# Kernel optimization log

Hardware: AMD Instinct MI355X
Metric: run time of the kernel (lower is better)

## Reference

```python
import jax, jax.numpy as jnp
import numpy as np

H = 8  # n_heads from init_kwargs
EPS = 1e-5


def _ln(x, g, b):
    m = jnp.mean(x, axis=-1, keepdims=True)
    v = jnp.mean((x - m) ** 2, axis=-1, keepdims=True)
    return (x - m) * jax.lax.rsqrt(v + EPS) * g + b


def setup_inputs() -> dict:
    key = jax.random.key(0)
    B, d_m, n, L, p_d = 1, 256, 128, 1024, 128
    ks = jax.random.split(key, 12)
    s = 0.02
    return {
        "msa": jax.random.normal(ks[0], (B, d_m, n, L), jnp.float32),
        "pairs": jax.random.normal(ks[1], (B, n, n, p_d), jnp.float32),
        "ln_m_g": jnp.ones((d_m,), jnp.float32),
        "ln_m_b": jnp.zeros((d_m,), jnp.float32),
        "ln_p_g": jnp.ones((p_d,), jnp.float32),
        "ln_p_b": jnp.zeros((p_d,), jnp.float32),
        "Wq": jax.random.normal(ks[2], (d_m, d_m), jnp.float32) * s,
        "Wk": jax.random.normal(ks[3], (d_m, d_m), jnp.float32) * s,
        "Wv": jax.random.normal(ks[4], (d_m, d_m), jnp.float32) * s,
        "Wg": jax.random.normal(ks[5], (d_m, d_m), jnp.float32) * s,
        "bg": jnp.zeros((d_m,), jnp.float32),
        "Wb": jax.random.normal(ks[6], (p_d, H), jnp.float32) * s,
        "Wo": jax.random.normal(ks[7], (d_m, d_m), jnp.float32) * s,
        "bo": jnp.zeros((d_m,), jnp.float32),
    }


def reference(msa, pairs, ln_m_g, ln_m_b, ln_p_g, ln_p_b,
              Wq, Wk, Wv, Wg, bg, Wb, Wo, bo):
    B, d_m, n, L = msa.shape
    dh = d_m // H
    sqrt_c = jnp.sqrt(jnp.asarray(dh, msa.dtype))

    x = _ln(jnp.transpose(msa, (0, 3, 2, 1)), ln_m_g, ln_m_b)      # [B,L,n,d_m]
    p = _ln(pairs, ln_p_g, ln_p_b)                                   # [B,n,n,p_d]

    # pair bias: (B,n,n,H) -> (B,1,H,n_q,n_k)
    bias = jnp.transpose(jnp.einsum('bijc,ch->bijh', p, Wb), (0, 3, 1, 2))[:, None]

    def heads(y):  # [B,L,n,d_m] -> [B,L,H,n,dh]
        return jnp.transpose(y.reshape(B, L, n, H, dh), (0, 1, 3, 2, 4))

    q = heads(x @ Wq)
    k = heads(x @ Wk)
    v = heads(x @ Wv)
    g = jax.nn.sigmoid(heads(x @ Wg + bg))

    scores = jnp.einsum('blhnd,blhmd->blhnm', q, k) / sqrt_c + bias  # [B,L,H,n,n]
    w = jax.nn.softmax(scores, axis=-1)
    attn = g * jnp.einsum('blhnm,blhmd->blhnd', w, v)                # [B,L,H,n,dh]

    attn = jnp.transpose(attn, (0, 1, 3, 2, 4)).reshape(B, L, n, d_m)
    out = attn @ Wo + bo                                             # [B,L,n,d_m]
    return jnp.transpose(out, (0, 3, 2, 1))                          # [B,d_m,n,L]
```

## Files before the change

kernel.cpp:

```cpp
#include <hip/hip_runtime.h>

__device__ __forceinline__ float bf_lo(unsigned u){ return __uint_as_float(u << 16); }
__device__ __forceinline__ float bf_hi(unsigned u){ return __uint_as_float(u & 0xffff0000u); }
__device__ __forceinline__ float bf1(unsigned short s){ return __uint_as_float((unsigned)s << 16); }
__device__ __forceinline__ unsigned short f2bf(float f){
  unsigned u = __float_as_uint(f);
  u += 0x7fffu + ((u >> 16) & 1u);
  return (unsigned short)(u >> 16);
}

typedef __attribute__((ext_vector_type(8))) short short8;
typedef __attribute__((ext_vector_type(4))) float f32x4;

__device__ __forceinline__ f32x4 mfma16(short8 a, short8 b, f32x4 c){
  return __builtin_amdgcn_mfma_f32_16x16x32_bf16(a, b, c, 0, 0, 0);
}

#define GLOAD_LDS16(g, l) \
  __builtin_amdgcn_global_load_lds((const __attribute__((address_space(1))) unsigned int*)(g), \
                                   (__attribute__((address_space(3))) unsigned int*)(l), 16, 0, 0)

__global__ __launch_bounds__(256) void ln_msa_kernel(
    const float* __restrict__ msa, const float* __restrict__ gam,
    const float* __restrict__ bet, unsigned short* __restrict__ x16)
{
  __shared__ float tile[256*33];
  __shared__ float ps[8*32], pq[8*32];
  __shared__ float mean_s[32], rstd_s[32];
  const int t = threadIdx.x;
  const int l0 = blockIdx.x * 32;
  const int n  = blockIdx.y;
  {
    const int lt = t & 31, ct = t >> 5;
    for (int r = 0; r < 32; ++r) {
      int c = r*8 + ct;
      tile[c*33 + lt] = msa[(size_t)c*131072 + (size_t)n*1024 + l0 + lt];
    }
  }
  __syncthreads();
  {
    const int lt = t & 31, cp = t >> 5;
    float s1 = 0.f, s2 = 0.f;
    for (int cc = 0; cc < 32; ++cc) {
      int c = cp*32 + ((cc + cp*4) & 31);
      float v = tile[c*33 + lt];
      s1 += v; s2 += v*v;
    }
    ps[cp*32 + lt] = s1; pq[cp*32 + lt] = s2;
  }
  __syncthreads();
  if (t < 32) {
    float s1 = 0.f, s2 = 0.f;
    for (int cp = 0; cp < 8; ++cp){ s1 += ps[cp*32+t]; s2 += pq[cp*32+t]; }
    float m = s1 * (1.f/256.f);
    float v = s2 * (1.f/256.f) - m*m;
    mean_s[t] = m;
    rstd_s[t] = rsqrtf(v + 1e-5f);
  }
  __syncthreads();
  {
    const float g = gam[t], b = bet[t];
    for (int l = 0; l < 32; ++l) {
      float v = (tile[t*33 + l] - mean_s[l]) * rstd_s[l] * g + b;
      x16[((size_t)(l0+l)*128 + n)*256 + t] = f2bf(v);
    }
  }
}

__global__ __launch_bounds__(64) void pair_bias_kernel(
    const float* __restrict__ pairs, const float* __restrict__ gam,
    const float* __restrict__ bet, const float* __restrict__ Wb,
    float* __restrict__ biasb)
{
  const int j = blockIdx.x, i = blockIdx.y;
  const int t = threadIdx.x;
  const float* row = pairs + ((size_t)i*128 + j)*128;
  float v0 = row[t], v1 = row[t+64];
  float s = v0 + v1;
  #pragma unroll
  for (int o = 1; o < 64; o <<= 1) s += __shfl_xor(s, o, 64);
  float m = s * (1.f/128.f);
  float d0 = v0 - m, d1 = v1 - m;
  float q = d0*d0 + d1*d1;
  #pragma unroll
  for (int o = 1; o < 64; o <<= 1) q += __shfl_xor(q, o, 64);
  float rstd = rsqrtf(q * (1.f/128.f) + 1e-5f);
  float n0 = d0 * rstd * gam[t]    + bet[t];
  float n1 = d1 * rstd * gam[t+64] + bet[t+64];
  #pragma unroll
  for (int h = 0; h < 8; ++h) {
    float p = n0 * Wb[t*8 + h] + n1 * Wb[(t+64)*8 + h];
    #pragma unroll
    for (int o = 1; o < 64; o <<= 1) p += __shfl_xor(p, o, 64);
    if (t == h) biasb[((size_t)h*128 + i)*128 + j] = p;
  }
}

__global__ __launch_bounds__(256) void wprep_kernel(
    const float* __restrict__ Wq, const float* __restrict__ Wk,
    const float* __restrict__ Wv, const float* __restrict__ Wg,
    const float* __restrict__ Wo,
    unsigned short* __restrict__ Wt, unsigned short* __restrict__ WoT)
{
  const int n = blockIdx.x, k = threadIdx.x;
  if (n < 1024) {
    const int mat = n >> 8, nl = n & 255;
    const float* W = (mat==0) ? Wq : (mat==1) ? Wk : (mat==2) ? Wv : Wg;
    float v = W[(size_t)k*256 + nl];
    if (mat == 0) v *= 0.17677669529663689f;
    Wt[(size_t)n*256 + k] = f2bf(v);
  } else {
    const int c = n - 1024;
    WoT[(size_t)c*256 + k] = f2bf(Wo[(size_t)k*256 + c]);
  }
}

__global__ __launch_bounds__(256) void qkvg_gemm(
    const unsigned short* __restrict__ X, const unsigned short* __restrict__ Wt,
    const float* __restrict__ bg, unsigned short* __restrict__ qkg,
    unsigned short* __restrict__ vT)
{
  __shared__ __align__(16) unsigned short As[128*64], Bs[128*64];
  const int t = threadIdx.x;
  const int m0 = blockIdx.x*128, n0 = blockIdx.y*128;
  const int w = t>>6, lane = t&63, fr = lane&15, quad = lane>>4;
  const int wm = (w>>1)*64, wn = (w&1)*64;
  f32x4 acc[4][4] = {};
  for (int k0 = 0; k0 < 256; k0 += 64) {
    if (k0) __syncthreads();
    #pragma unroll
    for (int pss = 0; pss < 4; ++pss) {
      int s = pss*256 + t;
      int row = s >> 3, pch = s & 7;
      int c = pch ^ (row & 7);
      const unsigned short* ga = X  + (size_t)(m0+row)*256 + k0 + c*8;
      const unsigned short* gb = Wt + (size_t)(n0+row)*256 + k0 + c*8;
      GLOAD_LDS16(ga, As + (s & ~63)*8);
      GLOAD_LDS16(gb, Bs + (s & ~63)*8);
    }
    __syncthreads();
    #pragma unroll
    for (int kt = 0; kt < 2; ++kt) {
      short8 af[4], bfr[4];
      #pragma unroll
      for (int mt=0;mt<4;++mt){ int r = wm+mt*16+fr; int ch = (kt*4+quad)^(r&7);
        af[mt] = *(const short8*)(As + r*64 + ch*8); }
      #pragma unroll
      for (int nt=0;nt<4;++nt){ int r = wn+nt*16+fr; int ch = (kt*4+quad)^(r&7);
        bfr[nt] = *(const short8*)(Bs + r*64 + ch*8); }
      #pragma unroll
      for (int mt=0;mt<4;++mt)
        #pragma unroll
        for (int nt=0;nt<4;++nt)
          acc[mt][nt] = mfma16(af[mt], bfr[nt], acc[mt][nt]);
    }
  }
  const int mat = n0 >> 8;
  #pragma unroll
  for (int mt=0;mt<4;++mt) {
    #pragma unroll
    for (int nt=0;nt<4;++nt) {
      const int ng = n0 + wn + nt*16 + fr;
      const int h = (ng>>5)&7, d = ng&31;
      #pragma unroll
      for (int reg=0;reg<4;++reg) {
        const int m = m0 + wm + mt*16 + quad*4 + reg;
        float v = acc[mt][nt][reg];
        if (mat == 3) v = 1.f/(1.f + __expf(-(v + bg[ng&255])));
        const unsigned short bv = f2bf(v);
        if (mat == 2) {
          const int ll = m>>7, nn = m&127;
          const int c = nn>>3, ph = c ^ (d&7);
          vT[((size_t)(h*1024 + ll))*4096 + d*128 + ph*8 + (nn&7)] = bv;
        } else {
          const int mi = ((mat==3)?2:mat)*8 + h;
          qkg[((size_t)mi*131072 + m)*32 + d] = bv;
        }
      }
    }
  }
}

__global__ __launch_bounds__(512) void attn_mfma(
    const unsigned short* __restrict__ qkg, const unsigned short* __restrict__ vT,
    const float* __restrict__ biasb, unsigned short* __restrict__ attn2)
{
  __shared__ __align__(16) unsigned short qs[128*32], ks[128*32], gs[128*32], vs[32*128];
  __shared__ __align__(16) unsigned short pbuf[8][16*136];
  const int t = threadIdx.x, l = blockIdx.x;
  const int w = t>>6, fr = t&15, quad = (t>>4)&3;
  unsigned short* pw = pbuf[w];
  const int rbase = w*16;
  const f32x4 zero4 = {0.f,0.f,0.f,0.f};
  for (int h = 0; h < 8; ++h) {
    {
      const unsigned short* g0 = qkg + ((size_t)(0*8+h)*131072 + (size_t)l*128)*32 + t*8;
      const unsigned short* g1 = qkg + ((size_t)(1*8+h)*131072 + (size_t)l*128)*32 + t*8;
      const unsigned short* g2 = qkg + ((size_t)(2*8+h)*131072 + (size_t)l*128)*32 + t*8;
      const unsigned short* g3 = vT  + ((size_t)(h*1024 + l))*4096 + t*8;
      const int lb = (t & ~63)*8;
      GLOAD_LDS16(g0, qs + lb);
      GLOAD_LDS16(g1, ks + lb);
      GLOAD_LDS16(g2, gs + lb);
      GLOAD_LDS16(g3, vs + lb);
    }
    __syncthreads();
    short8 aq = *(const short8*)(qs + (rbase+fr)*32 + quad*8);
    f32x4 S[8];
    #pragma unroll
    for (int nt=0;nt<8;++nt) {
      short8 bk = *(const short8*)(ks + (nt*16+fr)*32 + quad*8);
      S[nt] = mfma16(aq, bk, zero4);
    }
    const float* bb = biasb + ((size_t)h*128 + rbase + quad*4)*128 + fr;
    #pragma unroll
    for (int nt=0;nt<8;++nt)
      #pragma unroll
      for (int reg=0;reg<4;++reg)
        S[nt][reg] += bb[(size_t)reg*128 + nt*16];
    float mx[4] = {-1e30f,-1e30f,-1e30f,-1e30f};
    #pragma unroll
    for (int nt=0;nt<8;++nt)
      #pragma unroll
      for (int reg=0;reg<4;++reg) mx[reg] = fmaxf(mx[reg], S[nt][reg]);
    #pragma unroll
    for (int reg=0;reg<4;++reg) {
      mx[reg] = fmaxf(mx[reg], __shfl_xor(mx[reg], 1, 64));
      mx[reg] = fmaxf(mx[reg], __shfl_xor(mx[reg], 2, 64));
      mx[reg] = fmaxf(mx[reg], __shfl_xor(mx[reg], 4, 64));
      mx[reg] = fmaxf(mx[reg], __shfl_xor(mx[reg], 8, 64));
    }
    float sum[4] = {0.f,0.f,0.f,0.f};
    #pragma unroll
    for (int nt=0;nt<8;++nt)
      #pragma unroll
      for (int reg=0;reg<4;++reg) {
        float e = __expf(S[nt][reg]-mx[reg]);
        S[nt][reg] = e; sum[reg] += e;
      }
    #pragma unroll
    for (int reg=0;reg<4;++reg) {
      sum[reg] += __shfl_xor(sum[reg], 1, 64);
      sum[reg] += __shfl_xor(sum[reg], 2, 64);
      sum[reg] += __shfl_xor(sum[reg], 4, 64);
      sum[reg] += __shfl_xor(sum[reg], 8, 64);
    }
    float inv[4];
    #pragma unroll
    for (int reg=0;reg<4;++reg) inv[reg] = 1.f/sum[reg];
    #pragma unroll
    for (int nt=0;nt<8;++nt)
      #pragma unroll
      for (int reg=0;reg<4;++reg)
        pw[(quad*4+reg)*136 + nt*16 + fr] = f2bf(S[nt][reg]*inv[reg]);
    __builtin_amdgcn_s_waitcnt(0);
    f32x4 o[2] = {zero4, zero4};
    #pragma unroll
    for (int kt=0;kt<4;++kt) {
      short8 ap = *(const short8*)(pw + fr*136 + kt*32 + quad*8);
      #pragma unroll
      for (int n2=0;n2<2;++n2) {
        const int d = n2*16 + fr;
        const int ph = (kt*4+quad) ^ (d&7);
        short8 bv = *(const short8*)(vs + d*128 + ph*8);
        o[n2] = mfma16(ap, bv, o[n2]);
      }
    }
    #pragma unroll
    for (int n2=0;n2<2;++n2)
      #pragma unroll
      for (int reg=0;reg<4;++reg) {
        const int row = rbase + quad*4 + reg, col = n2*16 + fr;
        const float gv = bf1(gs[row*32 + col]);
        attn2[((size_t)row*1024 + l)*256 + h*32 + col] = f2bf(o[n2][reg]*gv);
      }
    __syncthreads();
  }
}

__global__ __launch_bounds__(256) void outproj_mfma(
    const unsigned short* __restrict__ attn2, const unsigned short* __restrict__ WoT,
    const float* __restrict__ bo, float* __restrict__ out)
{
  __shared__ __align__(16) unsigned short As[128*64], Bs[128*64];
  const int t = threadIdx.x;
  const int c0 = blockIdx.x*128;
  const int l0 = blockIdx.y*128;
  const int n  = blockIdx.z;
  const int w = t>>6, lane = t&63, fr = lane&15, quad = lane>>4;
  const int wm = (w>>1)*64, wn = (w&1)*64;
  f32x4 acc[4][4] = {};
  for (int k0 = 0; k0 < 256; k0 += 64) {
    if (k0) __syncthreads();
    #pragma unroll
    for (int pss = 0; pss < 4; ++pss) {
      int s = pss*256 + t;
      int row = s >> 3, pch = s & 7;
      int c = pch ^ (row & 7);
      const unsigned short* ga = WoT   + (size_t)(c0+row)*256 + k0 + c*8;
      const unsigned short* gb = attn2 + ((size_t)n*1024 + l0 + row)*256 + k0 + c*8;
      GLOAD_LDS16(ga, As + (s & ~63)*8);
      GLOAD_LDS16(gb, Bs + (s & ~63)*8);
    }
    __syncthreads();
    #pragma unroll
    for (int kt = 0; kt < 2; ++kt) {
      short8 af[4], bfr[4];
      #pragma unroll
      for (int mt=0;mt<4;++mt){ int r = wm+mt*16+fr; int ch = (kt*4+quad)^(r&7);
        af[mt] = *(const short8*)(As + r*64 + ch*8); }
      #pragma unroll
      for (int nt=0;nt<4;++nt){ int r = wn+nt*16+fr; int ch = (kt*4+quad)^(r&7);
        bfr[nt] = *(const short8*)(Bs + r*64 + ch*8); }
      #pragma unroll
      for (int mt=0;mt<4;++mt)
        #pragma unroll
        for (int nt=0;nt<4;++nt)
          acc[mt][nt] = mfma16(af[mt], bfr[nt], acc[mt][nt]);
    }
  }
  #pragma unroll
  for (int mt=0;mt<4;++mt) {
    #pragma unroll
    for (int reg=0;reg<4;++reg) {
      const int c = c0 + wm + mt*16 + quad*4 + reg;
      const float bv = bo[c];
      #pragma unroll
      for (int nt=0;nt<4;++nt) {
        const int l = l0 + wn + nt*16 + fr;
        out[(size_t)c*131072 + (size_t)n*1024 + l] = acc[mt][nt][reg] + bv;
      }
    }
  }
}

extern "C" void kernel_launch(void* const* d_in, const int* in_sizes, int n_in,
                              void* d_out, int out_size, void* d_ws, size_t ws_size,
                              hipStream_t stream) {
  const float* msa    = (const float*)d_in[0];
  const float* pairs  = (const float*)d_in[1];
  const float* ln_m_g = (const float*)d_in[2];
  const float* ln_m_b = (const float*)d_in[3];
  const float* ln_p_g = (const float*)d_in[4];
  const float* ln_p_b = (const float*)d_in[5];
  const float* Wq     = (const float*)d_in[6];
  const float* Wk     = (const float*)d_in[7];
  const float* Wv     = (const float*)d_in[8];
  const float* Wg     = (const float*)d_in[9];
  const float* bg     = (const float*)d_in[10];
  const float* Wb     = (const float*)d_in[11];
  const float* Wo     = (const float*)d_in[12];
  const float* bo     = (const float*)d_in[13];
  float* out = (float*)d_out;

  char* ws = (char*)d_ws;
  unsigned short* qkg  = (unsigned short*)(ws);
  unsigned short* vT   = (unsigned short*)(ws + (size_t)201326592);
  unsigned short* x16  = (unsigned short*)(ws + (size_t)268435456);
  float*          biasb= (float*)         (ws + (size_t)335544320);
  unsigned short* Wt   = (unsigned short*)(ws + (size_t)336068608);
  unsigned short* WoT  = (unsigned short*)(ws + (size_t)336592896);

  hipLaunchKernelGGL(ln_msa_kernel, dim3(32,128), dim3(256), 0, stream,
                     msa, ln_m_g, ln_m_b, x16);
  hipLaunchKernelGGL(pair_bias_kernel, dim3(128,128), dim3(64), 0, stream,
                     pairs, ln_p_g, ln_p_b, Wb, biasb);
  hipLaunchKernelGGL(wprep_kernel, dim3(1280), dim3(256), 0, stream,
                     Wq, Wk, Wv, Wg, Wo, Wt, WoT);
  hipLaunchKernelGGL(qkvg_gemm, dim3(1024,8), dim3(256), 0, stream,
                     x16, Wt, bg, qkg, vT);
  hipLaunchKernelGGL(attn_mfma, dim3(1024), dim3(512), 0, stream,
                     qkg, vT, biasb, x16);
  hipLaunchKernelGGL(outproj_mfma, dim3(2,8,128), dim3(256), 0, stream,
                     x16, WoT, bo, out);
}
```

Baseline: 640.4 us.

## Fuse QKVG projection GEMM into attention kernel to avoid global round-trip

Merges the QKVG projection GEMM into the per-row attention kernel. Each block loads its 128x256 X tile into LDS once, then for each head computes the q/k/v/g slices with MFMA directly into shared memory, so the intermediate qkg/vT tensors are never written to or read from global memory. This removes roughly 256MB of intermediate traffic and one kernel launch. The cost is a large LDS footprint (160KB) that limits occupancy to one block per CU, per-head reloading of weight slices, and serialized GEMM-then-attention phases inside each block.

After: 554.9 us. -13.4%, faster.

```diff
diff --git a/kernel.cpp b/kernel.cpp
--- a/kernel.cpp
+++ b/kernel.cpp
@@ -1,12 +1,15 @@
 #include <hip/hip_runtime.h>
 
-__device__ __forceinline__ float bf_lo(unsigned u){ return __uint_as_float(u << 16); }
-__device__ __forceinline__ float bf_hi(unsigned u){ return __uint_as_float(u & 0xffff0000u); }
 __device__ __forceinline__ float bf1(unsigned short s){ return __uint_as_float((unsigned)s << 16); }
 __device__ __forceinline__ unsigned short f2bf(float f){
   unsigned u = __float_as_uint(f);
   u += 0x7fffu + ((u >> 16) & 1u);
   return (unsigned short)(u >> 16);
+}
+__device__ __forceinline__ unsigned cvt_pk_bf16(float a, float b){
+  unsigned r;
+  asm("v_cvt_pk_bf16_f32 %0, %1, %2" : "=v"(r) : "v"(a), "v"(b));
+  return r;
 }
 
 typedef __attribute__((ext_vector_type(8))) short short8;
@@ -115,96 +118,95 @@
   }
 }
 
-__global__ __launch_bounds__(256) void qkvg_gemm(
+__global__ __launch_bounds__(512) void fused_qkvg_attn(
     const unsigned short* __restrict__ X, const unsigned short* __restrict__ Wt,
-    const float* __restrict__ bg, unsigned short* __restrict__ qkg,
-    unsigned short* __restrict__ vT)
-{
-  __shared__ __align__(16) unsigned short As[128*64], Bs[128*64];
-  const int t = threadIdx.x;
-  const int m0 = blockIdx.x*128, n0 = blockIdx.y*128;
-  const int w = t>>6, lane = t&63, fr = lane&15, quad = lane>>4;
-  const int wm = (w>>1)*64, wn = (w&1)*64;
-  f32x4 acc[4][4] = {};
-  for (int k0 = 0; k0 < 256; k0 += 64) {
-    if (k0) __syncthreads();
-    #pragma unroll
-    for (int pss = 0; pss < 4; ++pss) {
-      int s = pss*256 + t;
-      int row = s >> 3, pch = s & 7;
-      int c = pch ^ (row & 7);
-      const unsigned short* ga = X  + (size_t)(m0+row)*256 + k0 + c*8;
-      const unsigned short* gb = Wt + (size_t)(n0+row)*256 + k0 + c*8;
-      GLOAD_LDS16(ga, As + (s & ~63)*8);
-      GLOAD_LDS16(gb, Bs + (s & ~63)*8);
-    }
-    __syncthreads();
-    #pragma unroll
-    for (int kt = 0; kt < 2; ++kt) {
-      short8 af[4], bfr[4];
-      #pragma unroll
-      for (int mt=0;mt<4;++mt){ int r = wm+mt*16+fr; int ch = (kt*4+quad)^(r&7);
-        af[mt] = *(const short8*)(As + r*64 + ch*8); }
-      #pragma unroll
-      for (int nt=0;nt<4;++nt){ int r = wn+nt*16+fr; int ch = (kt*4+quad)^(r&7);
-        bfr[nt] = *(const short8*)(Bs + r*64 + ch*8); }
-      #pragma unroll
-      for (int mt=0;mt<4;++mt)
-        #pragma unroll
-        for (int nt=0;nt<4;++nt)
-          acc[mt][nt] = mfma16(af[mt], bfr[nt], acc[mt][nt]);
-    }
-  }
-  const int mat = n0 >> 8;
-  #pragma unroll
-  for (int mt=0;mt<4;++mt) {
-    #pragma unroll
-    for (int nt=0;nt<4;++nt) {
-      const int ng = n0 + wn + nt*16 + fr;
-      const int h = (ng>>5)&7, d = ng&31;
-      #pragma unroll
-      for (int reg=0;reg<4;++reg) {
-        const int m = m0 + wm + mt*16 + quad*4 + reg;
-        float v = acc[mt][nt][reg];
-        if (mat == 3) v = 1.f/(1.f + __expf(-(v + bg[ng&255])));
-        const unsigned short bv = f2bf(v);
-        if (mat == 2) {
-          const int ll = m>>7, nn = m&127;
-          const int c = nn>>3, ph = c ^ (d&7);
-          vT[((size_t)(h*1024 + ll))*4096 + d*128 + ph*8 + (nn&7)] = bv;
-        } else {
-          const int mi = ((mat==3)?2:mat)*8 + h;
-          qkg[((size_t)mi*131072 + m)*32 + d] = bv;
-        }
-      }
-    }
-  }
-}
-
-__global__ __launch_bounds__(512) void attn_mfma(
-    const unsigned short* __restrict__ qkg, const unsigned short* __restrict__ vT,
-    const float* __restrict__ biasb, unsigned short* __restrict__ attn2)
-{
-  __shared__ __align__(16) unsigned short qs[128*32], ks[128*32], gs[128*32], vs[32*128];
-  __shared__ __align__(16) unsigned short pbuf[8][16*136];
+    const float* __restrict__ bg, const float* __restrict__ biasb,
+    unsigned short* __restrict__ attn2)
+{
+  __shared__ __align__(16) unsigned short lds[81920];
+  unsigned short* Xs  = lds;
+  unsigned short* Wst = lds + 32768;
+  unsigned short* qs  = lds + 65536;
+  unsigned short* ks  = lds + 69632;
+  unsigned short* vs  = lds + 73728;
+  unsigned short* gs  = lds + 77824;
+
   const int t = threadIdx.x, l = blockIdx.x;
   const int w = t>>6, fr = t&15, quad = (t>>4)&3;
-  unsigned short* pw = pbuf[w];
+  const int mat = w>>1, dh = (w&1)*16;
+  const int d0 = dh + quad*4;
+  unsigned short* pw = Wst + w*2176;
   const int rbase = w*16;
   const f32x4 zero4 = {0.f,0.f,0.f,0.f};
+
+  #pragma unroll
+  for (int s = 0; s < 8; ++s) {
+    int cid = s*512 + t;
+    int k0b = cid>>10, r = (cid>>3)&127, pch = cid&7;
+    int c = pch ^ (r&7);
+    const unsigned short* g = X + ((size_t)l*128 + r)*256 + k0b*64 + c*8;
+    GLOAD_LDS16(g, Xs + (cid & ~63)*8);
+  }
+
   for (int h = 0; h < 8; ++h) {
-    {
-      const unsigned short* g0 = qkg + ((size_t)(0*8+h)*131072 + (size_t)l*128)*32 + t*8;
-      const unsigned short* g1 = qkg + ((size_t)(1*8+h)*131072 + (size_t)l*128)*32 + t*8;
-      const unsigned short* g2 = qkg + ((size_t)(2*8+h)*131072 + (size_t)l*128)*32 + t*8;
-      const unsigned short* g3 = vT  + ((size_t)(h*1024 + l))*4096 + t*8;
-      const int lb = (t & ~63)*8;
-      GLOAD_LDS16(g0, qs + lb);
-      GLOAD_LDS16(g1, ks + lb);
-      GLOAD_LDS16(g2, gs + lb);
-      GLOAD_LDS16(g3, vs + lb);
+    #pragma unroll
+    for (int s = 0; s < 8; ++s) {
+      int cid = s*512 + t;
+      int k0b = cid>>10, r = (cid>>3)&127, pch = cid&7;
+      int c = pch ^ (r&7);
+      const unsigned short* g = Wt + ((size_t)((r>>5)*256 + h*32 + (r&31)))*256 + k0b*64 + c*8;
+      GLOAD_LDS16(g, Wst + (cid & ~63)*8);
     }
     __syncthreads();
+
+    f32x4 acc[8] = {};
+    for (int k0 = 0; k0 < 4; ++k0) {
+      #pragma unroll
+      for (int kt = 0; kt < 2; ++kt) {
+        const int ck = kt*4 + quad;
+        const int lr = mat*32 + dh + fr;
+        short8 bf = *(const short8*)(Wst + k0*8192 + lr*64 + (ck^(lr&7))*8);
+        #pragma unroll
+        for (int mt = 0; mt < 8; ++mt) {
+          const int r = mt*16 + fr;
+          short8 af = *(const short8*)(Xs + k0*8192 + r*64 + (ck^(r&7))*8);
+          acc[mt] = mfma16(bf, af, acc[mt]);
+        }
+      }
+    }
+
+    if (mat == 2) {
+      #pragma unroll
+      for (int mt = 0; mt < 8; ++mt) {
+        const int m = mt*16 + fr;
+        #pragma unroll
+        for (int reg = 0; reg < 4; ++reg) {
+          const int d = d0 + reg;
+          vs[d*128 + (((m>>3)^(d&7))<<3) + (m&7)] = f2bf(acc[mt][reg]);
+        }
+      }
+    } else {
+      unsigned short* buf = (mat==0) ? qs : (mat==1) ? ks : gs;
+      float4 b4;
+      if (mat == 3) b4 = *(const float4*)(bg + h*32 + d0);
+      #pragma unroll
+      for (int mt = 0; mt < 8; ++mt) {
+        const int m = mt*16 + fr;
+        float v0 = acc[mt][0], v1 = acc[mt][1], v2 = acc[mt][2], v3 = acc[mt][3];
+        if (mat == 3) {
+          v0 = 1.f/(1.f + __expf(-(v0 + b4.x)));
+          v1 = 1.f/(1.f + __expf(-(v1 + b4.y)));
+          v2 = 1.f/(1.f + __expf(-(v2 + b4.z)));
+          v3 = 1.f/(1.f + __expf(-(v3 + b4.w)));
+        }
+        uint2 pk;
+        pk.x = cvt_pk_bf16(v0, v1);
+        pk.y = cvt_pk_bf16(v2, v3);
+        *(uint2*)(buf + m*32 + d0) = pk;
+      }
+    }
+    __syncthreads();
+
     short8 aq = *(const short8*)(qs + (rbase+fr)*32 + quad*8);
     f32x4 S[8];
     #pragma unroll
@@ -354,8 +356,7 @@
   float* out = (float*)d_out;
 
   char* ws = (char*)d_ws;
-  unsigned short* qkg  = (unsigned short*)(ws);
-  unsigned short* vT   = (unsigned short*)(ws + (size_t)201326592);
+  unsigned short* attn2= (unsigned short*)(ws);
   unsigned short* x16  = (unsigned short*)(ws + (size_t)268435456);
   float*          biasb= (float*)         (ws + (size_t)335544320);
   unsigned short* Wt   = (unsigned short*)(ws + (size_t)336068608);
@@ -367,10 +368,8 @@
                      pairs, ln_p_g, ln_p_b, Wb, biasb);
   hipLaunchKernelGGL(wprep_kernel, dim3(1280), dim3(256), 0, stream,
                      Wq, Wk, Wv, Wg, Wo, Wt, WoT);
-  hipLaunchKernelGGL(qkvg_gemm, dim3(1024,8), dim3(256), 0, stream,
-                     x16, Wt, bg, qkg, vT);
-  hipLaunchKernelGGL(attn_mfma, dim3(1024), dim3(512), 0, stream,
-                     qkg, vT, biasb, x16);
+  hipLaunchKernelGGL(fused_qkvg_attn, dim3(1024), dim3(512), 0, stream,
+                     x16, Wt, bg, biasb, attn2);
   hipLaunchKernelGGL(outproj_mfma, dim3(2,8,128), dim3(256), 0, stream,
-                     x16, WoT, bo, out);
-}
+                     attn2, WoT, bo, out);
+}
```
